# Kernel tuning notes

Hardware: AMD Instinct MI355X
Metric: run time of the kernel (lower is better)

## Reference

```python
import jax, jax.numpy as jnp
import numpy as np

FEAT_STRIDE = 16
PRE_NMS = 6000
POST_NMS = 300
NMS_THRESH = 0.7
NEG_THR = 0.3
POS_THR = 0.7
RPN_BATCH = 256
FG_FRAC = 0.5
SCALES = (8, 16, 32)
RATIOS = (0.5, 1.0, 2.0)
A = len(SCALES) * len(RATIOS)  # 9


def _generate_anchors():
    base = 16.0
    ctr = (base - 1.0) * 0.5
    size = base * base
    out = []
    for r in RATIOS:
        ws = np.round(np.sqrt(size / r))
        hs = np.round(ws * r)
        for s in SCALES:
            W = ws * s
            H = hs * s
            out.append([ctr - 0.5 * (W - 1), ctr - 0.5 * (H - 1),
                        ctr + 0.5 * (W - 1), ctr + 0.5 * (H - 1)])
    return np.array(out, np.float32)  # [9,4]


def _conv(x, w, b, pad):
    y = jax.lax.conv_general_dilated(x, w, (1, 1), [(pad, pad), (pad, pad)],
                                     dimension_numbers=('NCHW', 'OIHW', 'NCHW'))
    return y + b[None, :, None, None]


def _all_anchors(H, W):
    base = jnp.asarray(_generate_anchors())
    sx = jnp.arange(W, dtype=jnp.float32) * FEAT_STRIDE
    sy = jnp.arange(H, dtype=jnp.float32) * FEAT_STRIDE
    gy, gx = jnp.meshgrid(sy, sx, indexing='ij')
    shifts = jnp.stack([gx, gy, gx, gy], -1).reshape(-1, 1, 4)  # [H*W,1,4]
    return (shifts + base[None]).reshape(-1, 4)  # (h,w,a) order, [H*W*A,4]


def _decode(anchors, deltas):
    w = anchors[:, 2] - anchors[:, 0] + 1.0
    h = anchors[:, 3] - anchors[:, 1] + 1.0
    cx = anchors[:, 0] + 0.5 * w
    cy = anchors[:, 1] + 0.5 * h
    pcx = deltas[:, 0] * w + cx
    pcy = deltas[:, 1] * h + cy
    pw = jnp.exp(deltas[:, 2]) * w
    ph = jnp.exp(deltas[:, 3]) * h
    return jnp.stack([pcx - 0.5 * pw, pcy - 0.5 * ph, pcx + 0.5 * pw, pcy + 0.5 * ph], -1)


def _encode(anchors, gt):
    ew = anchors[:, 2] - anchors[:, 0] + 1.0
    eh = anchors[:, 3] - anchors[:, 1] + 1.0
    ecx = anchors[:, 0] + 0.5 * ew
    ecy = anchors[:, 1] + 0.5 * eh
    gw = gt[:, 2] - gt[:, 0] + 1.0
    gh = gt[:, 3] - gt[:, 1] + 1.0
    gcx = gt[:, 0] + 0.5 * gw
    gcy = gt[:, 1] + 0.5 * gh
    return jnp.stack([(gcx - ecx) / ew, (gcy - ecy) / eh,
                      jnp.log(gw / ew), jnp.log(gh / eh)], -1)


def _nms(boxes, scores, thresh, max_out):
    x1, y1, x2, y2 = boxes[:, 0], boxes[:, 1], boxes[:, 2], boxes[:, 3]
    areas = (x2 - x1 + 1.0) * (y2 - y1 + 1.0)
    N = boxes.shape[0]

    def body(k, st):
        valid, sel, selv = st
        s = jnp.where(valid, scores, -jnp.inf)
        i = jnp.argmax(s)
        ok = s[i] > -jnp.inf
        iw = jnp.maximum(jnp.minimum(x2[i], x2) - jnp.maximum(x1[i], x1) + 1.0, 0.0)
        ih = jnp.maximum(jnp.minimum(y2[i], y2) - jnp.maximum(y1[i], y1) + 1.0, 0.0)
        inter = iw * ih
        iou = inter / (areas[i] + areas - inter)
        valid = valid & (iou <= thresh)
        return valid, sel.at[k].set(i.astype(jnp.int32)), selv.at[k].set(ok)

    st = jax.lax.fori_loop(0, max_out, body,
                           (jnp.ones(N, bool), jnp.zeros(max_out, jnp.int32), jnp.zeros(max_out, bool)))
    return st[1], st[2]


def _propose_one(scores, deltas, anchors, imh, imw):
    boxes = _decode(anchors, deltas)
    boxes = jnp.stack([jnp.clip(boxes[:, 0], 0.0, imw - 1.0),
                       jnp.clip(boxes[:, 1], 0.0, imh - 1.0),
                       jnp.clip(boxes[:, 2], 0.0, imw - 1.0),
                       jnp.clip(boxes[:, 3], 0.0, imh - 1.0)], -1)
    top_s, idx = jax.lax.top_k(scores, PRE_NMS)
    top_b = boxes[idx]
    sel, selv = _nms(top_b, top_s, NMS_THRESH, POST_NMS)
    return top_b[sel] * selv[:, None].astype(top_b.dtype)  # [POST_NMS,4], zero rows when exhausted


def _anchor_target_one(gt, imh, imw, rfg, rbg, anchors):
    N = anchors.shape[0]
    ax1, ay1, ax2, ay2 = anchors[:, 0], anchors[:, 1], anchors[:, 2], anchors[:, 3]
    inside = (ax1 >= 0) & (ay1 >= 0) & (ax2 < imw) & (ay2 < imh)
    gx1, gy1, gx2, gy2 = gt[:, 0], gt[:, 1], gt[:, 2], gt[:, 3]
    gw = gx2 - gx1 + 1.0
    gh = gy2 - gy1 + 1.0
    gt_valid = ~((gw == 1.0) & (gh == 1.0))  # all-zero padded gt boxes
    aw = ax2 - ax1 + 1.0
    ah = ay2 - ay1 + 1.0
    iw = jnp.maximum(jnp.minimum(ax2[:, None], gx2[None, :]) - jnp.maximum(ax1[:, None], gx1[None, :]) + 1.0, 0.0)
    ih = jnp.maximum(jnp.minimum(ay2[:, None], gy2[None, :]) - jnp.maximum(ay1[:, None], gy1[None, :]) + 1.0, 0.0)
    inter = iw * ih
    iou = inter / ((aw * ah)[:, None] + (gw * gh)[None, :] - inter)  # [N,K]
    iou = jnp.where(gt_valid[None, :], iou, 0.0)
    iou = jnp.where(inside[:, None], iou, -1.0)  # outside anchors excluded, as in original
    max_ov = iou.max(1)
    arg = iou.argmax(1)
    gt_max = iou.max(0)
    gt_max = jnp.where(gt_max <= 0.0, 1e-5, gt_max)
    keep = (iou == gt_max[None, :]).any(1)  # anchors with max overlap per gt -> fg
    labels = jnp.full(N, -1.0, jnp.float32)
    labels = jnp.where(max_ov < NEG_THR, 0.0, labels)
    labels = jnp.where(keep, 1.0, labels)
    labels = jnp.where(max_ov >= POS_THR, 1.0, labels)
    labels = jnp.where(inside, labels, -1.0)

    def ranks(r, mask):
        order = jnp.argsort(jnp.where(mask, r, 2.0))
        return jnp.zeros(N, jnp.int32).at[order].set(jnp.arange(N, dtype=jnp.int32))

    num_fg = int(FG_FRAC * RPN_BATCH)
    fg_keep = (labels == 1.0) & (ranks(rfg, labels == 1.0) < num_fg)
    num_bg = RPN_BATCH - fg_keep.sum()
    bg_keep = (labels == 0.0) & (ranks(rbg, labels == 0.0) < num_bg)
    labels = jnp.where(fg_keep, 1.0, jnp.where(bg_keep, 0.0, -1.0))
    targets = _encode(anchors, gt[arg, :4])
    ones4 = jnp.ones((1, 4), jnp.float32)
    in_w = (labels == 1.0).astype(jnp.float32)[:, None] * ones4
    n_ex = (labels >= 0).sum().astype(jnp.float32)
    out_w = jnp.where(labels >= 0, 1.0 / n_ex, 0.0)[:, None] * ones4
    return labels, targets, in_w, out_w


def _rpn_forward(base_feat, im_info, gt_boxes, conv_w, conv_b, cls_w, cls_b, bbox_w, bbox_b):
    B, _, H, W = base_feat.shape
    x = jax.nn.relu(_conv(base_feat, conv_w, conv_b, 1))
    cls_score = _conv(x, cls_w, cls_b, 0)                 # [B,2A,H,W]
    # reshape(x,2) -> softmax over axis 1 -> reshape back
    prob = jax.nn.softmax(cls_score.reshape(B, 2, A * H, W), axis=1).reshape(B, 2 * A, H, W)
    bbox_pred = _conv(x, bbox_w, bbox_b, 0)               # [B,4A,H,W]
    anchors = _all_anchors(H, W)                          # [H*W*A,4]

    # ---- proposal layer (detached in original) ----
    fg = prob[:, A:, :, :].transpose(0, 2, 3, 1).reshape(B, -1)        # (h,w,a)
    deltas = bbox_pred.transpose(0, 2, 3, 1).reshape(B, -1, 4)
    rois_boxes = jax.vmap(_propose_one, in_axes=(0, 0, None, 0, 0))(
        jax.lax.stop_gradient(fg), jax.lax.stop_gradient(deltas), anchors, im_info[:, 0], im_info[:, 1])
    batch_idx = jnp.broadcast_to(jnp.arange(B, dtype=rois_boxes.dtype)[:, None, None], (B, POST_NMS, 1))
    rois = jnp.concatenate([batch_idx, rois_boxes], -1)   # [B,POST_NMS,5]

    # ---- anchor target layer (training path) ----
    key = jax.random.key(42)
    rfg = jax.random.uniform(key, (B, anchors.shape[0]))
    rbg = jax.random.uniform(jax.random.fold_in(key, 1), (B, anchors.shape[0]))
    labels, targets, in_w, out_w = jax.vmap(_anchor_target_one, in_axes=(0, 0, 0, 0, 0, None))(
        gt_boxes, im_info[:, 0], im_info[:, 1], rfg, rbg, anchors)
    # rearrange (h,w,a) -> (a,h,w) layouts to match torch permutes
    labels = labels.reshape(B, H, W, A).transpose(0, 3, 1, 2).reshape(B, -1)
    targets = targets.reshape(B, H, W, A * 4).transpose(0, 3, 1, 2)
    in_w = in_w.reshape(B, H, W, A * 4).transpose(0, 3, 1, 2)
    out_w = out_w.reshape(B, H, W, A * 4).transpose(0, 3, 1, 2)

    # cross-entropy over kept anchors
    logits = cls_score.reshape(B, 2, A, H, W).transpose(0, 2, 3, 4, 1).reshape(-1, 2)
    lab = labels.reshape(-1)
    m = (lab >= 0).astype(logits.dtype)
    logp = jax.nn.log_softmax(logits, axis=-1)
    idx = jnp.clip(lab, 0.0, 1.0).astype(jnp.int32)
    nll = -jnp.take_along_axis(logp, idx[:, None], axis=1)[:, 0]
    loss_cls = (nll * m).sum() / m.sum()

    # smooth-L1 box loss, sigma=3, sum dims [1,2,3] then mean over batch
    sigma2 = 9.0
    diff = in_w * (bbox_pred - targets)
    ad = jnp.abs(diff)
    flag = (ad < 1.0 / sigma2).astype(diff.dtype)
    lb = flag * 0.5 * sigma2 * diff * diff + (1.0 - flag) * (ad - 0.5 / sigma2)
    loss_box = (out_w * lb).sum(axis=(1, 2, 3)).mean()
    return rois, loss_cls, loss_box


def setup_inputs() -> dict:
    key = jax.random.key(0)
    ks = jax.random.split(key, 9)
    B, C, H, W = 4, 512, 50, 76
    base_feat = jax.random.normal(ks[0], (B, C, H, W), jnp.float32)
    conv_w = jax.random.normal(ks[1], (512, C, 3, 3), jnp.float32) * 0.01
    conv_b = jnp.zeros((512,), jnp.float32)
    cls_w = jax.random.normal(ks[2], (18, 512, 1, 1), jnp.float32) * 0.01
    cls_b = jnp.zeros((18,), jnp.float32)
    bbox_w = jax.random.normal(ks[3], (36, 512, 1, 1), jnp.float32) * 0.01
    bbox_b = jnp.zeros((36,), jnp.float32)
    imh, imw = float(H * FEAT_STRIDE), float(W * FEAT_STRIDE)
    im_info = jnp.tile(jnp.array([imh, imw, 1.0], jnp.float32), (B, 1))
    K = 20
    cx = jax.random.uniform(ks[4], (B, K)) * (imw - 100.0) + 50.0
    cy = jax.random.uniform(ks[5], (B, K)) * (imh - 100.0) + 50.0
    bw = jax.random.uniform(ks[6], (B, K)) * 270.0 + 30.0
    bh = jax.random.uniform(ks[7], (B, K)) * 270.0 + 30.0
    x1 = jnp.clip(cx - 0.5 * bw, 0.0, imw - 1.0)
    x2 = jnp.clip(cx + 0.5 * bw, 0.0, imw - 1.0)
    y1 = jnp.clip(cy - 0.5 * bh, 0.0, imh - 1.0)
    y2 = jnp.clip(cy + 0.5 * bh, 0.0, imh - 1.0)
    cls = jax.random.randint(ks[8], (B, K), 1, 21).astype(jnp.float32)
    gt_boxes = jnp.stack([x1, y1, x2, y2, cls], -1)
    num_boxes = jnp.full((B,), K, jnp.int32)
    return {"base_feat": base_feat, "im_info": im_info, "gt_boxes": gt_boxes,
            "num_boxes": num_boxes, "conv_w": conv_w, "conv_b": conv_b,
            "cls_w": cls_w, "cls_b": cls_b, "bbox_w": bbox_w, "bbox_b": bbox_b}


def reference(base_feat, im_info, gt_boxes, num_boxes, conv_w, conv_b, cls_w, cls_b, bbox_w, bbox_b):
    # num_boxes is implicitly handled via zero-padded gt_boxes (as in the original layer)
    return _rpn_forward(base_feat, im_info, gt_boxes, conv_w, conv_b, cls_w, cls_b, bbox_w, bbox_b)
```

## Files before the change

### kernel.cpp

```cpp
#include <hip/hip_runtime.h>
#include <stdint.h>

#define HHH 50
#define WWW 76
#define NPIX 3800
#define NA 34200
#define NSORT 65536
#define PRE 6000
#define POST 300
#define NW 94
#define CIN 512
#define COUT 512
#define NBATCH 4
#define NGT 20
#define TFHALF 68400u
#define PPLANE 4400
#define XTB 2252800

typedef __bf16 bf16x8 __attribute__((ext_vector_type(8)));
typedef float f32x4 __attribute__((ext_vector_type(4)));
typedef unsigned int u32x4v __attribute__((ext_vector_type(4)));

__device__ static inline f32x4 MFMA16(bf16x8 a, bf16x8 b, f32x4 c) {
  return __builtin_amdgcn_mfma_f32_16x16x32_bf16(a, b, c, 0, 0, 0);
}

__host__ __device__ static inline void tf2x32(unsigned k0, unsigned k1, unsigned& x0, unsigned& x1) {
  unsigned k2 = k0 ^ k1 ^ 0x1BD11BDAu;
#define TFR(r) do { x0 += x1; x1 = (x1 << (r)) | (x1 >> (32 - (r))); x1 ^= x0; } while (0)
  x0 += k0; x1 += k1;
  TFR(13); TFR(15); TFR(26); TFR(6);
  x0 += k1; x1 += k2 + 1u;
  TFR(17); TFR(29); TFR(16); TFR(24);
  x0 += k2; x1 += k0 + 2u;
  TFR(13); TFR(15); TFR(26); TFR(6);
  x0 += k0; x1 += k1 + 3u;
  TFR(17); TFR(29); TFR(16); TFR(24);
  x0 += k1; x1 += k2 + 4u;
  TFR(13); TFR(15); TFR(26); TFR(6);
  x0 += k2; x1 += k0 + 5u;
#undef TFR
}

__device__ static inline unsigned tf_u23(unsigned k0, unsigned k1, unsigned p) {
  unsigned x0, x1;
  if (p < TFHALF) { x0 = p; x1 = p + TFHALF; tf2x32(k0, k1, x0, x1); return x0 >> 9; }
  x0 = p - TFHALF; x1 = p; tf2x32(k0, k1, x0, x1); return x1 >> 9;
}

__device__ const float BA[9][4] = {
  {-84.f, -40.f,  99.f,  55.f}, {-176.f, -88.f, 191.f, 103.f}, {-360.f, -184.f, 375.f, 199.f},
  {-56.f, -56.f,  71.f,  71.f}, {-120.f, -120.f, 135.f, 135.f}, {-248.f, -248.f, 263.f, 263.f},
  {-36.f, -80.f,  51.f,  95.f}, {-80.f, -168.f,  95.f, 183.f}, {-168.f, -344.f, 183.f, 359.f}
};

__device__ static inline unsigned monoF(float f) {
  int b = __float_as_int(f);
  unsigned u = (unsigned)b;
  return (b < 0) ? ~u : (u | 0x80000000u);
}
__device__ static inline float unmonoF(unsigned u) {
  unsigned b = (u & 0x80000000u) ? (u ^ 0x80000000u) : ~u;
  return __int_as_float((int)b);
}

__device__ static inline void split3(float v, unsigned short& h, unsigned short& m, unsigned short& l) {
  __bf16 b0 = (__bf16)v;  float f0 = (float)b0;
  float r = v - f0;       __bf16 b1 = (__bf16)r;  float f1 = (float)b1;
  float r2 = r - f1;      __bf16 b2 = (__bf16)r2;
  h = __builtin_bit_cast(unsigned short, b0);
  m = __builtin_bit_cast(unsigned short, b1);
  l = __builtin_bit_cast(unsigned short, b2);
}

__global__ void k_init(unsigned* gtmaxU, int* cnts, float* accums) {
  int t = threadIdx.x;
  if (t < NBATCH * NGT) gtmaxU[t] = 0x407FFFFFu;
  if (t < 8) cnts[t] = 0;
  if (t < 8) accums[t] = 0.f;
}

__global__ void k_split_x(const float* __restrict__ feat, unsigned short* __restrict__ x0,
                          unsigned short* __restrict__ x1, unsigned short* __restrict__ x2) {
  int tid = blockIdx.x * 256 + threadIdx.x;
  if (tid >= NBATCH * XTB) return;
  int b = tid / XTB;
  int rem = tid - b * XTB;
  int pg = rem >> 13;
  int r2 = rem & 8191;
  int cg = r2 >> 7;
  int po = (r2 >> 3) & 15;
  int cl = r2 & 7;
  int ci = cg * 8 + cl;
  int px = pg * 16 + po;
  int hq = px / 80, wq = px - hq * 80;
  float v = 0.f;
  if (hq >= 2 && hq < 52 && wq >= 1 && wq < 77)
    v = feat[((size_t)(b * 512 + ci)) * NPIX + (hq - 2) * 76 + (wq - 1)];
  unsigned short h, m, l;
  split3(v, h, m, l);
  x0[tid] = h; x1[tid] = m; x2[tid] = l;
}

__global__ void k_split_w(const float* __restrict__ cw, unsigned short* __restrict__ w0,
                          unsigned short* __restrict__ w1, unsigned short* __restrict__ w2) {
  int tid = blockIdx.x * 256 + threadIdx.x;
  if (tid >= 9 * 64 * 512 * 8) return;
  int cl = tid & 7;
  int co = (tid >> 3) & 511;
  int cg = (tid >> 12) & 63;
  int tap = tid >> 18;
  int ci = cg * 8 + cl;
  float v = cw[((size_t)co * 512 + ci) * 9 + tap];
  unsigned short h, m, l;
  split3(v, h, m, l);
  w0[tid] = h; w1[tid] = m; w2[tid] = l;
}

__global__ void k_tr_w1(const float* __restrict__ clsw, const float* __restrict__ bbw, float* __restrict__ wt1) {
  int tid = blockIdx.x * 256 + threadIdx.x;
  if (tid >= CIN * 64) return;
  int c = tid & 63, ci = tid >> 6;
  float v = 0.f;
  if (c < 18) v = clsw[c * 512 + ci];
  else if (c < 54) v = bbw[(c - 18) * 512 + ci];
  wt1[tid] = v;
}

__global__ __launch_bounds__(256, 2) void k_conv3(
    const unsigned short* __restrict__ XT0, const unsigned short* __restrict__ XT1,
    const unsigned short* __restrict__ XT2,
    const unsigned short* __restrict__ WT0, const unsigned short* __restrict__ WT1,
    const unsigned short* __restrict__ WT2,
    const float* __restrict__ bias, float* __restrict__ out) {
  const int d = blockIdx.x;
  const int copair = (d >> 1) & 3, half = d & 1, g = d >> 3;
  const int cob = copair * 2 + (g & 1);
  const int pxb = half * 64 + (g >> 1);
  const int pxp = pxb & 31, b = pxb >> 5;
  const int co0 = cob * 64;
  const int px0 = 160 + pxp * 128;
  const int t = threadIdx.x, l = t & 63, wv = t >> 6;
  const int wr = wv >> 1, wc = wv & 1;
  const int l15 = l & 15, lq = l >> 4;
  __shared__ __align__(16) unsigned short WL[2][3][4][64][8];
  __shared__ float biasL[64];
  if (t < 64) biasL[t] = bias[co0 + t];
  f32x4 cmain[2][4], ccorr[2][4];
  double accd[2][4][4];
#pragma unroll
  for (int c = 0; c < 2; ++c)
#pragma unroll
    for (int p = 0; p < 4; ++p) {
      cmain[c][p] = (f32x4)(0.f); ccorr[c][p] = (f32x4)(0.f);
#pragma unroll
      for (int r = 0; r < 4; ++r) accd[c][p][r] = 0.0;
    }
  const unsigned short* xt0 = XT0 + (size_t)b * XTB;
  const unsigned short* xt1 = XT1 + (size_t)b * XTB;
  const unsigned short* xt2 = XT2 + (size_t)b * XTB;
  const unsigned short* wts[3] = {WT0, WT1, WT2};
  const int t63 = t & 63;

  u32x4v st0, st1, st2;
#define GLOAD(s)                                                                       \
  do {                                                                                 \
    int tap_ = (s) >> 4, k0g_ = ((s) & 15) << 2;                                       \
    int e0 = t, e1 = 256 + t, e2 = 512 + t;                                            \
    st0 = *(const u32x4v*)(wts[0] + (size_t)(((tap_ * 64 + k0g_ + ((e0 >> 6) & 3)) * 512 + co0 + t63)) * 8); \
    st1 = *(const u32x4v*)(wts[1] + (size_t)(((tap_ * 64 + k0g_ + ((e1 >> 6) & 3)) * 512 + co0 + t63)) * 8); \
    st2 = *(const u32x4v*)(wts[2] + (size_t)(((tap_ * 64 + k0g_ + ((e2 >> 6) & 3)) * 512 + co0 + t63)) * 8); \
  } while (0)
#define SWRITE(buf)                                                                    \
  do {                                                                                 \
    unsigned short* base_ = &WL[buf][0][0][0][0];                                      \
    *(u32x4v*)(base_ + (size_t)t * 8) = st0;                                           \
    *(u32x4v*)(base_ + (size_t)(256 + t) * 8) = st1;                                   \
    *(u32x4v*)(base_ + (size_t)(512 + t) * 8) = st2;                                   \
  } while (0)

  GLOAD(0);
  SWRITE(0);
  __syncthreads();
  const int coA = wr * 32 + l15;
  for (int s = 0; s < 144; ++s) {
    const int tap = s >> 4;
    const int dh = tap / 3, dw = tap - dh * 3;
    const int off = (dh - 1) * 80 + (dw - 1);
    const int cb = s & 1, nb = cb ^ 1;
    if (s < 143) GLOAD(s + 1);
    bf16x8 A[2][3];
#pragma unroll
    for (int c = 0; c < 2; ++c)
#pragma unroll
      for (int sp = 0; sp < 3; ++sp)
        A[c][sp] = __builtin_bit_cast(bf16x8, *(const u32x4v*)&WL[cb][sp][lq][coA + c * 16][0]);
    const int cgl = (s & 15) * 4 + lq;
    const int pxbase = px0 + wc * 64 + off + l15;
#pragma unroll
    for (int p = 0; p < 4; ++p) {
      const int px = pxbase + p * 16;
      const size_t eo = (size_t)((px >> 4) * 8192 + cgl * 128 + (px & 15) * 8);
      bf16x8 B0 = __builtin_bit_cast(bf16x8, *(const u32x4v*)(xt0 + eo));
      bf16x8 B1 = __builtin_bit_cast(bf16x8, *(const u32x4v*)(xt1 + eo));
      bf16x8 B2 = __builtin_bit_cast(bf16x8, *(const u32x4v*)(xt2 + eo));
#pragma unroll
      for (int c = 0; c < 2; ++c) {
        cmain[c][p] = MFMA16(A[c][0], B0, cmain[c][p]);
        ccorr[c][p] = MFMA16(A[c][2], B0, ccorr[c][p]);
        ccorr[c][p] = MFMA16(A[c][0], B2, ccorr[c][p]);
        ccorr[c][p] = MFMA16(A[c][1], B1, ccorr[c][p]);
        ccorr[c][p] = MFMA16(A[c][1], B0, ccorr[c][p]);
        ccorr[c][p] = MFMA16(A[c][0], B1, ccorr[c][p]);
      }
    }
    if ((s & 3) == 3) {
#pragma unroll
      for (int c = 0; c < 2; ++c)
#pragma unroll
        for (int p = 0; p < 4; ++p) {
#pragma unroll
          for (int r = 0; r < 4; ++r) accd[c][p][r] += (double)cmain[c][p][r];
          cmain[c][p] = (f32x4)(0.f);
        }
    }
    if (s < 143) SWRITE(nb);
    __syncthreads();
  }
#undef GLOAD
#undef SWRITE
  const size_t outb = ((size_t)b * 512 + co0) * NPIX;
#pragma unroll
  for (int c = 0; c < 2; ++c)
#pragma unroll
    for (int p = 0; p < 4; ++p)
#pragma unroll
      for (int r = 0; r < 4; ++r) {
        int coL = wr * 32 + c * 16 + lq * 4 + r;
        int px = px0 + wc * 64 + p * 16 + l15;
        int hq = px / 80, wq = px - hq * 80;
        if (hq >= 2 && hq < 52 && wq >= 1 && wq < 77) {
          float v = (float)(accd[c][p][r] + (double)ccorr[c][p][r]) + biasL[coL];
          out[outb + (size_t)coL * NPIX + (hq - 2) * 76 + (wq - 1)] = fmaxf(v, 0.f);
        }
      }
}

__global__ __launch_bounds__(256) void k_conv1(const float* __restrict__ x, const float* __restrict__ wt1,
                                               const float* __restrict__ clsb, const float* __restrict__ bbb,
                                               float* __restrict__ clsS, float* __restrict__ bbp) {
  const int b = blockIdx.y;
  const int px0 = blockIdx.x * 128;
  const int t = threadIdx.x;
  const int cg = t & 7, pg = t >> 3;
  __shared__ float xs[16][128];
  __shared__ float ws[16][72];
  double acc[8][4];
#pragma unroll
  for (int i = 0; i < 8; ++i)
#pragma unroll
    for (int j = 0; j < 4; ++j) acc[i][j] = 0.0;
  const float* xb = x + (size_t)b * CIN * NPIX;
  for (int cc = 0; cc < CIN; cc += 16) {
#pragma unroll
    for (int e0 = 0; e0 < 8; ++e0) {
      int e = t + e0 * 256;
      int r = e >> 7, c = e & 127;
      int p = px0 + c;
      xs[r][c] = (p < NPIX) ? xb[(size_t)(cc + r) * NPIX + p] : 0.f;
    }
#pragma unroll
    for (int e0 = 0; e0 < 4; ++e0) {
      int e = t + e0 * 256;
      int r = e >> 6, c = e & 63;
      ws[r][c + ((c >> 5) << 2)] = wt1[(cc + r) * 64 + c];
    }
    __syncthreads();
    const int wcol = (cg << 3) + ((cg >> 2) << 2);
    const int xcol = pg << 2;
    float a32[8][4];
#pragma unroll
    for (int i = 0; i < 8; ++i)
#pragma unroll
      for (int j = 0; j < 4; ++j) a32[i][j] = 0.f;
#pragma unroll
    for (int k = 0; k < 16; ++k) {
      const float4 w0 = *(const float4*)&ws[k][wcol];
      const float4 w1 = *(const float4*)&ws[k][wcol + 4];
      const float4 xa = *(const float4*)&xs[k][xcol];
      const float wv[8] = {w0.x, w0.y, w0.z, w0.w, w1.x, w1.y, w1.z, w1.w};
      const float xv[4] = {xa.x, xa.y, xa.z, xa.w};
#pragma unroll
      for (int i = 0; i < 8; ++i)
#pragma unroll
        for (int j = 0; j < 4; ++j)
          a32[i][j] = fmaf(wv[i], xv[j], a32[i][j]);
    }
#pragma unroll
    for (int i = 0; i < 8; ++i)
#pragma unroll
      for (int j = 0; j < 4; ++j) acc[i][j] += (double)a32[i][j];
    __syncthreads();
  }
#pragma unroll
  for (int i = 0; i < 8; ++i) {
    int c = cg * 8 + i;
#pragma unroll
    for (int j = 0; j < 4; ++j) {
      int p = px0 + pg * 4 + j;
      if (p < NPIX) {
        if (c < 18) clsS[((size_t)b * 18 + c) * NPIX + p] = (float)acc[i][j] + clsb[c];
        else if (c < 54) bbp[((size_t)b * 36 + (c - 18)) * NPIX + p] = (float)acc[i][j] + bbb[c - 18];
      }
    }
  }
}

__global__ void k_decode(const float* __restrict__ clsS, const float* __restrict__ bbp,
                         const float* __restrict__ im_info, float* __restrict__ boxes,
                         unsigned long long* __restrict__ keys) {
  int tid = blockIdx.x * 256 + threadIdx.x;
  int b = tid >> 16, n = tid & 0xFFFF;
  if (n >= NA) { keys[((size_t)b << 16) + n] = 0ull; return; }
  int a = n % 9, p = n / 9;
  int h = p / WWW, w = p - h * WWW;
  const float* cb = clsS + (size_t)b * 18 * NPIX;
  float s0 = cb[(size_t)a * NPIX + p];
  float s1 = cb[(size_t)(9 + a) * NPIX + p];
  float mx = fmaxf(s0, s1);
  float e0 = expf(s0 - mx), e1 = expf(s1 - mx);
  float fg = e1 / (e0 + e1);
  const float* bb = bbp + (size_t)b * 36 * NPIX;
  float d0 = bb[(size_t)(a * 4 + 0) * NPIX + p];
  float d1 = bb[(size_t)(a * 4 + 1) * NPIX + p];
  float d2 = bb[(size_t)(a * 4 + 2) * NPIX + p];
  float d3 = bb[(size_t)(a * 4 + 3) * NPIX + p];
  float ax1 = BA[a][0] + w * 16.f, ay1 = BA[a][1] + h * 16.f;
  float ax2 = BA[a][2] + w * 16.f, ay2 = BA[a][3] + h * 16.f;
  float aw = ax2 - ax1 + 1.f, ah = ay2 - ay1 + 1.f;
  float acx = ax1 + 0.5f * aw, acy = ay1 + 0.5f * ah;
  float pcx = d0 * aw + acx, pcy = d1 * ah + acy;
  float pw = expf(d2) * aw, ph = expf(d3) * ah;
  float imh = im_info[b * 3 + 0], imw = im_info[b * 3 + 1];
  float x1 = fminf(fmaxf(pcx - 0.5f * pw, 0.f), imw - 1.f);
  float y1 = fminf(fmaxf(pcy - 0.5f * ph, 0.f), imh - 1.f);
  float x2 = fminf(fmaxf(pcx + 0.5f * pw, 0.f), imw - 1.f);
  float y2 = fminf(fmaxf(pcy + 0.5f * ph, 0.f), imh - 1.f);
  float* bx = boxes + ((size_t)b * NA + n) * 4;
  bx[0] = x1; bx[1] = y1; bx[2] = x2; bx[3] = y2;
  unsigned fb = __float_as_uint(fg);
  keys[((size_t)b << 16) + n] = ((unsigned long long)fb << 32) | (unsigned)(~(unsigned)n);
}

__global__ __launch_bounds__(256) void k_sort_local0(unsigned long long* keys) {
  __shared__ unsigned long long s[2048];
  const int chunk = blockIdx.x;
  const int b = chunk >> 5, cloc = chunk & 31;
  unsigned long long* base = keys + ((size_t)b << 16) + ((size_t)cloc << 11);
  const int gbase = cloc << 11;
  const int t = threadIdx.x;
  for (int e = t; e < 2048; e += 256) s[e] = base[e];
  __syncthreads();
  for (int k = 2; k <= 2048; k <<= 1) {
    for (int j = k >> 1; j >= 1; j >>= 1) {
      for (int q = t; q < 1024; q += 256) {
        int i = ((q & ~(j - 1)) << 1) | (q & (j - 1));
        int pp = i | j;
        bool up = (((unsigned)(gbase + i)) & (unsigned)k) == 0;
        unsigned long long a = s[i], dd = s[pp];
        if (up ? (a < dd) : (a > dd)) { s[i] = dd; s[pp] = a; }
      }
      __syncthreads();
    }
  }
  for (int e = t; e < 2048; e += 256) base[e] = s[e];
}
__global__ __launch_bounds__(256) void k_sort_merge(unsigned long long* keys, int k) {
  __shared__ unsigned long long s[2048];
  const int chunk = blockIdx.x;
  const int b = chunk >> 5, cloc = chunk & 31;
  unsigned long long* base = keys + ((size_t)b << 16) + ((size_t)cloc << 11);
  const int gbase = cloc << 11;
  const int t = threadIdx.x;
  for (int e = t; e < 2048; e += 256) s[e] = base[e];
  __syncthreads();
  for (int j = 1024; j >= 1; j >>= 1) {
    for (int q = t; q < 1024; q += 256) {
      int i = ((q & ~(j - 1)) << 1) | (q & (j - 1));
      int pp = i | j;
      bool up = (((unsigned)(gbase + i)) & (unsigned)k) == 0;
      unsigned long long a = s[i], dd = s[pp];
      if (up ? (a < dd) : (a > dd)) { s[i] = dd; s[pp] = a; }
    }
    __syncthreads();
  }
  for (int e = t; e < 2048; e += 256) base[e] = s[e];
}
__global__ void k_sort_gstep(unsigned long long* keys, int k, int j) {
  int tid = blockIdx.x * 256 + threadIdx.x;
  int b = tid >> 16, i = tid & 0xFFFF;
  if ((i & j) != 0) return;
  int pp = i | j;
  unsigned long long* base = keys + ((size_t)b << 16);
  unsigned long long a = base[i], dd = base[pp];
  bool up = (((unsigned)i) & (unsigned)k) == 0;
  if (up ? (a < dd) : (a > dd)) { base[i] = dd; base[pp] = a; }
}

__global__ void k_gather(const unsigned long long* __restrict__ keys, const float* __restrict__ boxes,
                         float* tbx1, float* tby1, float* tbx2, float* tby2, float* tba) {
  int tid = blockIdx.x * 256 + threadIdx.x;
  if (tid >= NBATCH * PRE) return;
  int b = tid / PRE;
  int k = tid - b * PRE;
  unsigned long long key = keys[((size_t)b << 16) + k];
  unsigned n = ~(unsigned)(key & 0xFFFFFFFFu);
  const float* bx = boxes + ((size_t)b * NA + n) * 4;
  float x1 = bx[0], y1 = bx[1], x2 = bx[2], y2 = bx[3];
  tbx1[tid] = x1; tby1[tid] = y1; tbx2[tid] = x2; tby2[tid] = y2;
  tba[tid] = (x2 - x1 + 1.f) * (y2 - y1 + 1.f);
}

__global__ __launch_bounds__(256) void k_mask(const float* __restrict__ tbx1, const float* __restrict__ tby1,
                                              const float* __restrict__ tbx2, const float* __restrict__ tby2,
                                              const float* __restrict__ tba, unsigned long long* __restrict__ mask) {
  const int b = blockIdx.y;
  const int i0 = blockIdx.x * 64;
  const int t = threadIdx.x;
  __shared__ float jx1[2048], jy1[2048], jx2[2048], jy2[2048], ja[2048];
  __shared__ float ix1[64], iy1[64], ix2[64], iy2[64], ia[64];
  const float* bx1 = tbx1 + b * PRE;
  const float* by1 = tby1 + b * PRE;
  const float* bx2 = tbx2 + b * PRE;
  const float* by2 = tby2 + b * PRE;
  const float* ba2 = tba + b * PRE;
  if (t < 64) {
    int i = i0 + t;
    if (i < PRE) { ix1[t] = bx1[i]; iy1[t] = by1[i]; ix2[t] = bx2[i]; iy2[t] = by2[i]; ia[t] = ba2[i]; }
    else { ix1[t] = 0; iy1[t] = 0; ix2[t] = 0; iy2[t] = 0; ia[t] = 1; }
  }
  for (int c = 0; c < 3; ++c) {
    int j0 = c * 2048;
    for (int e = t; e < 2048; e += 256) {
      int j = j0 + e;
      if (j < PRE) { jx1[e] = bx1[j]; jy1[e] = by1[j]; jx2[e] = bx2[j]; jy2[e] = by2[j]; ja[e] = ba2[j]; }
      else { jx1[e] = 0; jy1[e] = 0; jx2[e] = 0; jy2[e] = 0; ja[e] = 1; }
    }
    __syncthreads();
    for (int task = t; task < 64 * 32; task += 256) {
      int il = task & 63, wl = task >> 6;
      int i = i0 + il;
      int wg = (j0 >> 6) + wl;
      if (i >= PRE || wg >= NW) continue;
      unsigned long long word = 0ull;
      float X1 = ix1[il], Y1 = iy1[il], X2 = ix2[il], Y2 = iy2[il], A = ia[il];
      for (int l = 0; l < 64; ++l) {
        int j = wg * 64 + l;
        if (j > i && j < PRE) {
          int e = j - j0;
          float iw = fminf(X2, jx2[e]) - fmaxf(X1, jx1[e]) + 1.f;
          float ih = fminf(Y2, jy2[e]) - fmaxf(Y1, jy1[e]) + 1.f;
          if (iw > 0.f && ih > 0.f) {
            float inter = iw * ih;
            float iou = inter / (A + ja[e] - inter);
            if (iou > 0.7f) word |= (1ull << l);
          }
        }
      }
      mask[((size_t)(b * PRE + i)) * NW + wg] = word;
    }
    __syncthreads();
  }
}

__global__ void k_nms(const unsigned long long* __restrict__ mask,
                      const float* __restrict__ tbx1, const float* __restrict__ tby1,
                      const float* __restrict__ tbx2, const float* __restrict__ tby2,
                      float* __restrict__ out) {
  const int b = blockIdx.x;
  const int lane = threadIdx.x;
  __shared__ unsigned long long rem[NW];
  for (int w = lane; w < NW; w += 64) rem[w] = 0ull;
  __syncthreads();
  int sc = 0;
  for (int w = 0; w < NW && sc < POST; ++w) {
    while (sc < POST) {
      unsigned long long avail = ~rem[w];
      if (w == NW - 1) avail &= (1ull << (PRE - (NW - 1) * 64)) - 1ull;
      if (avail == 0ull) break;
      int l = __ffsll((unsigned long long)avail) - 1;
      int j = w * 64 + l;
      if (lane < 5) {
        float v;
        if (lane == 0) v = (float)b;
        else if (lane == 1) v = tbx1[b * PRE + j];
        else if (lane == 2) v = tby1[b * PRE + j];
        else if (lane == 3) v = tbx2[b * PRE + j];
        else v = tby2[b * PRE + j];
        out[((size_t)(b * POST + sc)) * 5 + lane] = v;
      }
      sc++;
      if (sc == POST) break;
      const unsigned long long* row = mask + ((size_t)(b * PRE + j)) * NW;
      for (int w2 = w + lane; w2 < NW; w2 += 64) {
        unsigned long long m = row[w2];
        if (w2 == w) m |= (1ull << l);
        rem[w2] |= m;
      }
      __syncthreads();
    }
  }
  for (int r2 = sc; r2 < POST; ++r2)
    if (lane < 5) out[((size_t)(b * POST + r2)) * 5 + lane] = (lane == 0) ? (float)b : 0.f;
}

__global__ __launch_bounds__(256) void k_iouA(const float* __restrict__ gt_boxes, const float* __restrict__ im_info,
                                              float* __restrict__ iou, float* __restrict__ maxov,
                                              int* __restrict__ argm, unsigned* __restrict__ gtmaxU) {
  const int b = blockIdx.y;
  const int n = blockIdx.x * 256 + threadIdx.x;
  __shared__ float g[NGT][6];
  if (threadIdx.x < NGT) {
    const float* gg = gt_boxes + (b * NGT + threadIdx.x) * 5;
    float x1 = gg[0], y1 = gg[1], x2 = gg[2], y2 = gg[3];
    g[threadIdx.x][0] = x1; g[threadIdx.x][1] = y1; g[threadIdx.x][2] = x2; g[threadIdx.x][3] = y2;
    float gw = x2 - x1 + 1.f, gh = y2 - y1 + 1.f;
    g[threadIdx.x][4] = gw * gh;
    g[threadIdx.x][5] = ((gw == 1.f) && (gh == 1.f)) ? 0.f : 1.f;
  }
  __syncthreads();
  if (n >= NA) return;
  int a = n % 9, p = n / 9;
  int h = p / WWW, w = p - h * WWW;
  float ax1 = BA[a][0] + w * 16.f, ay1 = BA[a][1] + h * 16.f;
  float ax2 = BA[a][2] + w * 16.f, ay2 = BA[a][3] + h * 16.f;
  float imh = im_info[b * 3 + 0], imw = im_info[b * 3 + 1];
  bool inside = (ax1 >= 0.f) && (ay1 >= 0.f) && (ax2 < imw) && (ay2 < imh);
  float aw = ax2 - ax1 + 1.f, ah = ay2 - ay1 + 1.f;
  float aa = aw * ah;
  float best = -2.f;
  int barg = 0;
  float* row = iou + ((size_t)(b * NA) + n) * NGT;
#pragma unroll
  for (int j = 0; j < NGT; ++j) {
    float iw = fmaxf(fminf(ax2, g[j][2]) - fmaxf(ax1, g[j][0]) + 1.f, 0.f);
    float ih = fmaxf(fminf(ay2, g[j][3]) - fmaxf(ay1, g[j][1]) + 1.f, 0.f);
    float inter = iw * ih;
    float v = inter / (aa + g[j][4] - inter);
    if (g[j][5] == 0.f) v = 0.f;
    if (!inside) v = -1.f;
    row[j] = v;
    if (v > best) { best = v; barg = j; }
    if (v > 0.f) atomicMax(&gtmaxU[b * NGT + j], monoF(v));
  }
  maxov[b * NA + n] = best;
  argm[b * NA + n] = barg;
}

__global__ __launch_bounds__(256) void k_labels(const float* __restrict__ iou, const float* __restrict__ maxov,
                                                const unsigned* __restrict__ gtmaxU, const float* __restrict__ im_info,
                                                unsigned kf0, unsigned kf1, unsigned kb0, unsigned kb1,
                                                int* __restrict__ labels, unsigned* __restrict__ ufg,
                                                unsigned* __restrict__ ubg, int* __restrict__ cnts) {
  const int b = blockIdx.y;
  const int n = blockIdx.x * 256 + threadIdx.x;
  __shared__ float gmf[NGT];
  if (threadIdx.x < NGT) {
    float gm = unmonoF(gtmaxU[b * NGT + threadIdx.x]);
    gmf[threadIdx.x] = (gm <= 0.f) ? 1e-5f : gm;
  }
  __syncthreads();
  int label = -1;
  if (n < NA) {
    int a = n % 9, p = n / 9;
    int h = p / WWW, w = p - h * WWW;
    float ax1 = BA[a][0] + w * 16.f, ay1 = BA[a][1] + h * 16.f;
    float ax2 = BA[a][2] + w * 16.f, ay2 = BA[a][3] + h * 16.f;
    float imh = im_info[b * 3 + 0], imw = im_info[b * 3 + 1];
    bool inside = (ax1 >= 0.f) && (ay1 >= 0.f) && (ax2 < imw) && (ay2 < imh);
    float mo = maxov[b * NA + n];
    const float* row = iou + ((size_t)(b * NA) + n) * NGT;
    bool keep = false;
#pragma unroll
    for (int j = 0; j < NGT; ++j) keep = keep || (row[j] == gmf[j]);
    if (mo < 0.3f) label = 0;
    if (keep) label = 1;
    if (mo >= 0.7f) label = 1;
    if (!inside) label = -1;
    labels[b * NA + n] = label;
    unsigned pp = (unsigned)(b * NA + n);
    ufg[b * NA + n] = (label == 1) ? tf_u23(kf0, kf1, pp) : 0xFFFFFFFFu;
    ubg[b * NA + n] = (label == 0) ? tf_u23(kb0, kb1, pp) : 0xFFFFFFFFu;
  }
  unsigned long long bf = __ballot(label == 1);
  unsigned long long bb = __ballot(label == 0);
  if ((threadIdx.x & 63) == 0) {
    atomicAdd(&cnts[b], (int)__popcll(bf));
    atomicAdd(&cnts[4 + b], (int)__popcll(bb));
  }
}

__global__ __launch_bounds__(1024) void k_select(const unsigned* __restrict__ ufg, const unsigned* __restrict__ ubg,
                                                 const int* __restrict__ cnts, unsigned* __restrict__ selp,
                                                 float* __restrict__ nexf) {
  const int blk = blockIdx.x;
  const int b = blk >> 1, cls = blk & 1;
  const unsigned* u = (cls == 0 ? ufg : ubg) + (size_t)b * NA;
  const int fcnt = cnts[b], bcnt = cnts[4 + b];
  const int kk = (cls == 0) ? 128 : (256 - (fcnt < 128 ? fcnt : 128));
  const int cnt = (cls == 0) ? fcnt : bcnt;
  __shared__ int partial[16];
  __shared__ int s_cnt;
  auto bcount = [&](auto pred) -> int {
    int c = 0;
    for (int i = threadIdx.x; i < NA; i += 1024) c += pred((unsigned)i, u[i]) ? 1 : 0;
    for (int o = 32; o > 0; o >>= 1) c += __shfl_down(c, o);
    if ((threadIdx.x & 63) == 0) partial[threadIdx.x >> 6] = c;
    __syncthreads();
    if (threadIdx.x == 0) { int s = 0; for (int q = 0; q < 16; ++q) s += partial[q]; s_cnt = s; }
    __syncthreads();
    int r = s_cnt;
    __syncthreads();
    return r;
  };
  unsigned thr, ithr;
  if (cnt <= kk) { thr = 0xFFFFFFFFu; ithr = 0xFFFFFFFFu; }
  else {
    unsigned lo = 0, hi = 0x00800000u;
    while (lo < hi) {
      unsigned mid = lo + ((hi - lo) >> 1);
      int c = bcount([&](unsigned, unsigned v) { return v <= mid; });
      if (c >= kk) hi = mid; else lo = mid + 1;
    }
    thr = lo;
    int c1 = (thr == 0u) ? 0 : bcount([&](unsigned, unsigned v) { return v < thr; });
    int need = kk - c1;
    unsigned lo2 = 0, hi2 = NA - 1;
    while (lo2 < hi2) {
      unsigned mid = lo2 + ((hi2 - lo2) >> 1);
      int c = bcount([&](unsigned i, unsigned v) { return (v == thr) && (i <= mid); });
      if (c >= need) hi2 = mid; else lo2 = mid + 1;
    }
    ithr = lo2;
  }
  if (threadIdx.x == 0) {
    selp[blk * 2] = thr;
    selp[blk * 2 + 1] = ithr;
    if (cls == 1) {
      int fk = fcnt < 128 ? fcnt : 128;
      int bk2 = bcnt < kk ? bcnt : kk;
      nexf[b] = (float)(fk + bk2);
    }
  }
}

__global__ __launch_bounds__(256) void k_loss(const float* __restrict__ clsS, const float* __restrict__ bbp,
                                              const float* __restrict__ gt_boxes, const int* __restrict__ labels,
                                              const unsigned* __restrict__ ufg, const unsigned* __restrict__ ubg,
                                              const unsigned* __restrict__ selp, const int* __restrict__ argm,
                                              float* __restrict__ accums) {
  const int b = blockIdx.y;
  const int n = blockIdx.x * 256 + threadIdx.x;
  float nll = 0.f, mcnt = 0.f, lbsum = 0.f;
  if (n < NA) {
    int label = labels[b * NA + n];
    int fin = -1;
    if (label == 1) {
      unsigned uu = ufg[b * NA + n];
      unsigned thr = selp[(b * 2 + 0) * 2], ithr = selp[(b * 2 + 0) * 2 + 1];
      if (uu < thr || (uu == thr && (unsigned)n <= ithr)) fin = 1;
    } else if (label == 0) {
      unsigned uu = ubg[b * NA + n];
      unsigned thr = selp[(b * 2 + 1) * 2], ithr = selp[(b * 2 + 1) * 2 + 1];
      if (uu < thr || (uu == thr && (unsigned)n <= ithr)) fin = 0;
    }
    if (fin >= 0) {
      int a = n % 9, p = n / 9;
      float s0 = clsS[((size_t)b * 18 + a) * NPIX + p];
      float s1 = clsS[((size_t)b * 18 + 9 + a) * NPIX + p];
      float mx = fmaxf(s0, s1);
      float lse = mx + logf(expf(s0 - mx) + expf(s1 - mx));
      nll = lse - (fin == 1 ? s1 : s0);
      mcnt = 1.f;
      if (fin == 1) {
        int h = p / WWW, w = p - h * WWW;
        float ax1 = BA[a][0] + w * 16.f, ay1 = BA[a][1] + h * 16.f;
        float ax2 = BA[a][2] + w * 16.f, ay2 = BA[a][3] + h * 16.f;
        float ew = ax2 - ax1 + 1.f, eh = ay2 - ay1 + 1.f;
        float ecx = ax1 + 0.5f * ew, ecy = ay1 + 0.5f * eh;
        int ag = argm[b * NA + n];
        const float* gg = gt_boxes + (b * NGT + ag) * 5;
        float gw = gg[2] - gg[0] + 1.f, gh = gg[3] - gg[1] + 1.f;
        float gcx = gg[0] + 0.5f * gw, gcy = gg[1] + 0.5f * gh;
        float tt[4];
        tt[0] = (gcx - ecx) / ew;
        tt[1] = (gcy - ecy) / eh;
        tt[2] = logf(gw / ew);
        tt[3] = logf(gh / eh);
#pragma unroll
        for (int dd = 0; dd < 4; ++dd) {
          float pd = bbp[((size_t)b * 36 + (a * 4 + dd)) * NPIX + p];
          float diff = pd - tt[dd];
          float ad = fabsf(diff);
          lbsum += (ad < 1.f / 9.f) ? 4.5f * diff * diff : (ad - 0.5f / 9.f);
        }
      }
    }
  }
  for (int o = 32; o > 0; o >>= 1) {
    nll += __shfl_down(nll, o);
    mcnt += __shfl_down(mcnt, o);
    lbsum += __shfl_down(lbsum, o);
  }
  __shared__ float p0[4], p1[4], p2[4];
  int wid = threadIdx.x >> 6;
  if ((threadIdx.x & 63) == 0) { p0[wid] = nll; p1[wid] = mcnt; p2[wid] = lbsum; }
  __syncthreads();
  if (threadIdx.x == 0) {
    float aS = 0, bS = 0, cS = 0;
    for (int q = 0; q < 4; ++q) { aS += p0[q]; bS += p1[q]; cS += p2[q]; }
    atomicAdd(&accums[0], aS);
    atomicAdd(&accums[1], bS);
    atomicAdd(&accums[2 + b], cS);
  }
}

__global__ void k_final(const float* __restrict__ accums, const float* __restrict__ nexf, float* __restrict__ out) {
  if (threadIdx.x == 0 && blockIdx.x == 0) {
    out[6000] = accums[0] / accums[1];
    float lb = 0.f;
    for (int b = 0; b < NBATCH; ++b) lb += accums[2 + b] / nexf[b];
    out[6001] = lb * 0.25f;
  }
}

extern "C" void kernel_launch(void* const* d_in, const int* in_sizes, int n_in,
                              void* d_out, int out_size, void* d_ws, size_t ws_size,
                              hipStream_t stream) {
  (void)in_sizes; (void)n_in; (void)out_size; (void)ws_size;
  const float* base_feat = (const float*)d_in[0];
  const float* im_info   = (const float*)d_in[1];
  const float* gt_boxes  = (const float*)d_in[2];
  const float* conv_w    = (const float*)d_in[4];
  const float* conv_b    = (const float*)d_in[5];
  const float* cls_w     = (const float*)d_in[6];
  const float* cls_b     = (const float*)d_in[7];
  const float* bbox_w    = (const float*)d_in[8];
  const float* bbox_b    = (const float*)d_in[9];
  float* out = (float*)d_out;

  char* wp = (char*)d_ws;
  auto carve = [&](size_t bytes) -> void* {
    void* r = (void*)wp;
    wp += (bytes + 255) & ~(size_t)255;
    return r;
  };
  float* x     = (float*)carve((size_t)NBATCH * CIN * NPIX * 4);
  float* clsS  = (float*)carve((size_t)NBATCH * 18 * NPIX * 4);
  float* bbp   = (float*)carve((size_t)NBATCH * 36 * NPIX * 4);
  unsigned short* WT0 = (unsigned short*)carve((size_t)9 * 64 * 512 * 8 * 2);
  unsigned short* WT1 = (unsigned short*)carve((size_t)9 * 64 * 512 * 8 * 2);
  unsigned short* WT2 = (unsigned short*)carve((size_t)9 * 64 * 512 * 8 * 2);
  float* wt1   = (float*)carve((size_t)CIN * 64 * 4);
  unsigned* gtmaxU = (unsigned*)carve(NBATCH * NGT * 4);
  int* cnts    = (int*)carve(8 * 4);
  unsigned* selp = (unsigned*)carve(16 * 4);
  float* nexf  = (float*)carve(4 * 4);
  float* accums = (float*)carve(8 * 4);

  char* overlay = wp;
  unsigned short* XT0 = (unsigned short*)overlay;
  unsigned short* XT1 = XT0 + (size_t)NBATCH * XTB;
  unsigned short* XT2 = XT1 + (size_t)NBATCH * XTB;
  char* wp2 = overlay;
  auto carve2 = [&](size_t bytes) -> void* {
    void* r = (void*)wp2;
    wp2 += (bytes + 255) & ~(size_t)255;
    return r;
  };
  float* boxes = (float*)carve2((size_t)NBATCH * NA * 4 * 4);
  unsigned long long* keys = (unsigned long long*)carve2((size_t)NBATCH * NSORT * 8);
  float* tbx1 = (float*)carve2((size_t)NBATCH * PRE * 4);
  float* tby1 = (float*)carve2((size_t)NBATCH * PRE * 4);
  float* tbx2 = (float*)carve2((size_t)NBATCH * PRE * 4);
  float* tby2 = (float*)carve2((size_t)NBATCH * PRE * 4);
  float* tba  = (float*)carve2((size_t)NBATCH * PRE * 4);
  unsigned long long* mask = (unsigned long long*)carve2((size_t)NBATCH * PRE * NW * 8);
  float* iou   = (float*)carve2((size_t)NBATCH * NA * NGT * 4);
  float* maxov = (float*)carve2((size_t)NBATCH * NA * 4);
  int* argm    = (int*)carve2((size_t)NBATCH * NA * 4);
  int* labels  = (int*)carve2((size_t)NBATCH * NA * 4);
  unsigned* ufg = (unsigned*)carve2((size_t)NBATCH * NA * 4);
  unsigned* ubg = (unsigned*)carve2((size_t)NBATCH * NA * 4);

  unsigned kb0 = 0u, kb1 = 1u;
  tf2x32(0u, 42u, kb0, kb1);

  k_init<<<dim3(1), dim3(256), 0, stream>>>(gtmaxU, cnts, accums);
  k_split_w<<<dim3((9 * 64 * 512 * 8) / 256), dim3(256), 0, stream>>>(conv_w, WT0, WT1, WT2);
  k_tr_w1<<<dim3((CIN * 64) / 256), dim3(256), 0, stream>>>(cls_w, bbox_w, wt1);
  k_split_x<<<dim3((NBATCH * XTB + 255) / 256), dim3(256), 0, stream>>>(base_feat, XT0, XT1, XT2);
  k_conv3<<<dim3(1024), dim3(256), 0, stream>>>(XT0, XT1, XT2, WT0, WT1, WT2, conv_b, x);
  k_conv1<<<dim3(30, 4), dim3(256), 0, stream>>>(x, wt1, cls_b, bbox_b, clsS, bbp);
  k_decode<<<dim3(NBATCH * NSORT / 256), dim3(256), 0, stream>>>(clsS, bbp, im_info, boxes, keys);
  k_sort_local0<<<dim3(NBATCH * 32), dim3(256), 0, stream>>>(keys);
  for (int k = 4096; k <= 65536; k <<= 1) {
    for (int j = k >> 1; j >= 2048; j >>= 1)
      k_sort_gstep<<<dim3(NBATCH * NSORT / 256), dim3(256), 0, stream>>>(keys, k, j);
    k_sort_merge<<<dim3(NBATCH * 32), dim3(256), 0, stream>>>(keys, k);
  }
  k_gather<<<dim3((NBATCH * PRE + 255) / 256), dim3(256), 0, stream>>>(keys, boxes, tbx1, tby1, tbx2, tby2, tba);
  k_mask<<<dim3(NW, NBATCH), dim3(256), 0, stream>>>(tbx1, tby1, tbx2, tby2, tba, mask);
  k_nms<<<dim3(NBATCH), dim3(64), 0, stream>>>(mask, tbx1, tby1, tbx2, tby2, out);
  k_iouA<<<dim3((NA + 255) / 256, NBATCH), dim3(256), 0, stream>>>(gt_boxes, im_info, iou, maxov, argm, gtmaxU);
  k_labels<<<dim3((NA + 255) / 256, NBATCH), dim3(256), 0, stream>>>(iou, maxov, gtmaxU, im_info,
                                                                     0u, 42u, kb0, kb1, labels, ufg, ubg, cnts);
  k_select<<<dim3(8), dim3(1024), 0, stream>>>(ufg, ubg, cnts, selp, nexf);
  k_loss<<<dim3((NA + 255) / 256, NBATCH), dim3(256), 0, stream>>>(clsS, bbp, gt_boxes, labels, ufg, ubg, selp, argm, accums);
  k_final<<<dim3(1), dim3(1), 0, stream>>>(accums, nexf, out);
}
```

Before: 1.672 ms.

## Load conv weights directly from global, drop LDS staging and barriers

The 3x3 conv kernel no longer stages weight tiles through double-buffered shared memory with a __syncthreads per step. Each wave now loads its A fragments straight from global memory. The loop is reordered so channel groups are outer and the 9 taps are unrolled inside, and the double-precision flush now runs every 2 channel groups (18 tap-steps) rather than every 4 steps. This removes LDS traffic and block-wide barriers, at the cost of redundant global weight loads across waves and more register pressure from the unrolled taps.

```diff
diff --git a/kernel.cpp b/kernel.cpp
--- a/kernel.cpp
+++ b/kernel.cpp
@@ -23,6 +23,9 @@
 
 __device__ static inline f32x4 MFMA16(bf16x8 a, bf16x8 b, f32x4 c) {
   return __builtin_amdgcn_mfma_f32_16x16x32_bf16(a, b, c, 0, 0, 0);
+}
+__device__ static inline bf16x8 LD8(const unsigned short* p) {
+  return __builtin_bit_cast(bf16x8, *(const u32x4v*)p);
 }
 
 __host__ __device__ static inline void tf2x32(unsigned k0, unsigned k1, unsigned& x0, unsigned& x1) {
@@ -143,9 +146,6 @@
   const int t = threadIdx.x, l = t & 63, wv = t >> 6;
   const int wr = wv >> 1, wc = wv & 1;
   const int l15 = l & 15, lq = l >> 4;
-  __shared__ __align__(16) unsigned short WL[2][3][4][64][8];
-  __shared__ float biasL[64];
-  if (t < 64) biasL[t] = bias[co0 + t];
   f32x4 cmain[2][4], ccorr[2][4];
   double accd[2][4][4];
 #pragma unroll
@@ -159,62 +159,41 @@
   const unsigned short* xt0 = XT0 + (size_t)b * XTB;
   const unsigned short* xt1 = XT1 + (size_t)b * XTB;
   const unsigned short* xt2 = XT2 + (size_t)b * XTB;
-  const unsigned short* wts[3] = {WT0, WT1, WT2};
-  const int t63 = t & 63;
-
-  u32x4v st0, st1, st2;
-#define GLOAD(s)                                                                       \
-  do {                                                                                 \
-    int tap_ = (s) >> 4, k0g_ = ((s) & 15) << 2;                                       \
-    int e0 = t, e1 = 256 + t, e2 = 512 + t;                                            \
-    st0 = *(const u32x4v*)(wts[0] + (size_t)(((tap_ * 64 + k0g_ + ((e0 >> 6) & 3)) * 512 + co0 + t63)) * 8); \
-    st1 = *(const u32x4v*)(wts[1] + (size_t)(((tap_ * 64 + k0g_ + ((e1 >> 6) & 3)) * 512 + co0 + t63)) * 8); \
-    st2 = *(const u32x4v*)(wts[2] + (size_t)(((tap_ * 64 + k0g_ + ((e2 >> 6) & 3)) * 512 + co0 + t63)) * 8); \
-  } while (0)
-#define SWRITE(buf)                                                                    \
-  do {                                                                                 \
-    unsigned short* base_ = &WL[buf][0][0][0][0];                                      \
-    *(u32x4v*)(base_ + (size_t)t * 8) = st0;                                           \
-    *(u32x4v*)(base_ + (size_t)(256 + t) * 8) = st1;                                   \
-    *(u32x4v*)(base_ + (size_t)(512 + t) * 8) = st2;                                   \
-  } while (0)
-
-  GLOAD(0);
-  SWRITE(0);
-  __syncthreads();
   const int coA = wr * 32 + l15;
-  for (int s = 0; s < 144; ++s) {
-    const int tap = s >> 4;
-    const int dh = tap / 3, dw = tap - dh * 3;
-    const int off = (dh - 1) * 80 + (dw - 1);
-    const int cb = s & 1, nb = cb ^ 1;
-    if (s < 143) GLOAD(s + 1);
-    bf16x8 A[2][3];
-#pragma unroll
-    for (int c = 0; c < 2; ++c)
-#pragma unroll
-      for (int sp = 0; sp < 3; ++sp)
-        A[c][sp] = __builtin_bit_cast(bf16x8, *(const u32x4v*)&WL[cb][sp][lq][coA + c * 16][0]);
-    const int cgl = (s & 15) * 4 + lq;
-    const int pxbase = px0 + wc * 64 + off + l15;
-#pragma unroll
-    for (int p = 0; p < 4; ++p) {
-      const int px = pxbase + p * 16;
-      const size_t eo = (size_t)((px >> 4) * 8192 + cgl * 128 + (px & 15) * 8);
-      bf16x8 B0 = __builtin_bit_cast(bf16x8, *(const u32x4v*)(xt0 + eo));
-      bf16x8 B1 = __builtin_bit_cast(bf16x8, *(const u32x4v*)(xt1 + eo));
-      bf16x8 B2 = __builtin_bit_cast(bf16x8, *(const u32x4v*)(xt2 + eo));
-#pragma unroll
-      for (int c = 0; c < 2; ++c) {
-        cmain[c][p] = MFMA16(A[c][0], B0, cmain[c][p]);
-        ccorr[c][p] = MFMA16(A[c][2], B0, ccorr[c][p]);
-        ccorr[c][p] = MFMA16(A[c][0], B2, ccorr[c][p]);
-        ccorr[c][p] = MFMA16(A[c][1], B1, ccorr[c][p]);
-        ccorr[c][p] = MFMA16(A[c][1], B0, ccorr[c][p]);
-        ccorr[c][p] = MFMA16(A[c][0], B1, ccorr[c][p]);
+  const int OFFT[9] = {-81, -80, -79, -1, 0, 1, 79, 80, 81};
+  const int pxw = px0 + wc * 64 + l15;
+
+  for (int kg = 0; kg < 16; ++kg) {
+    const int cgl = kg * 4 + lq;
+    const int cglo = cgl * 128;
+    const size_t aro = ((size_t)cgl * 512 + co0 + coA) * 8;
+#pragma unroll
+    for (int tap = 0; tap < 9; ++tap) {
+      const size_t ao = aro + (size_t)tap * (64 * 512 * 8);
+      bf16x8 A0[2], A1[2], A2[2];
+      A0[0] = LD8(WT0 + ao); A0[1] = LD8(WT0 + ao + 128);
+      A1[0] = LD8(WT1 + ao); A1[1] = LD8(WT1 + ao + 128);
+      A2[0] = LD8(WT2 + ao); A2[1] = LD8(WT2 + ao + 128);
+      const int pxbase = pxw + OFFT[tap];
+      const size_t eob = (size_t)((pxbase >> 4) * 8192 + (pxbase & 15) * 8 + cglo);
+#pragma unroll
+      for (int p = 0; p < 4; ++p) {
+        const size_t eo = eob + (size_t)p * 8192;
+        bf16x8 B0 = LD8(xt0 + eo);
+        bf16x8 B1 = LD8(xt1 + eo);
+        bf16x8 B2 = LD8(xt2 + eo);
+#pragma unroll
+        for (int c = 0; c < 2; ++c) {
+          cmain[c][p] = MFMA16(A0[c], B0, cmain[c][p]);
+          ccorr[c][p] = MFMA16(A2[c], B0, ccorr[c][p]);
+          ccorr[c][p] = MFMA16(A0[c], B2, ccorr[c][p]);
+          ccorr[c][p] = MFMA16(A1[c], B1, ccorr[c][p]);
+          ccorr[c][p] = MFMA16(A1[c], B0, ccorr[c][p]);
+          ccorr[c][p] = MFMA16(A0[c], B1, ccorr[c][p]);
+        }
       }
     }
-    if ((s & 3) == 3) {
+    if (kg & 1) {
 #pragma unroll
       for (int c = 0; c < 2; ++c)
 #pragma unroll
@@ -224,11 +203,7 @@
           cmain[c][p] = (f32x4)(0.f);
         }
     }
-    if (s < 143) SWRITE(nb);
-    __syncthreads();
-  }
-#undef GLOAD
-#undef SWRITE
+  }
   const size_t outb = ((size_t)b * 512 + co0) * NPIX;
 #pragma unroll
   for (int c = 0; c < 2; ++c)
@@ -240,7 +215,7 @@
         int px = px0 + wc * 64 + p * 16 + l15;
         int hq = px / 80, wq = px - hq * 80;
         if (hq >= 2 && hq < 52 && wq >= 1 && wq < 77) {
-          float v = (float)(accd[c][p][r] + (double)ccorr[c][p][r]) + biasL[coL];
+          float v = (float)(accd[c][p][r] + (double)ccorr[c][p][r]) + bias[co0 + coL];
           out[outb + (size_t)coL * NPIX + (hq - 2) * 76 + (wq - 1)] = fmaxf(v, 0.f);
         }
       }
```

New measurement: 1.530 ms. -8.5%, faster.
